# Optimization experiments

Measured on AMD Instinct MI355X. Metric: run time of the kernel, lower is better.

The kernel has to match this reference:

```python
import jax, jax.numpy as jnp
import numpy as np

N = 16384   # nodes
K = 10      # knn_graph(k=11) minus self-loop -> 10 neighbors per node
H = 128     # hidden_nf
L = 7       # n_layers
IN = 8      # in_node_nf
OUT = 4     # out_node_nf


def setup_inputs() -> dict:
    key = jax.random.key(0)
    ks = jax.random.split(key, 20)
    s = 0.05
    rn = lambda k, shp, sc=s: (jax.random.normal(k, shp, dtype=jnp.float32) * sc)
    return {
        "h": jax.random.normal(ks[0], (N, 3 + IN), dtype=jnp.float32) * 100.0,  # cols 0:3 coords (divided by 3330 inside), 3: features
        "idx": jax.random.randint(ks[1], (N, K), 0, N),  # neighbor (src) indices per dst node
        "emb_in_w": rn(ks[2], (IN, H)), "emb_in_b": rn(ks[3], (H,)),
        "edge_w1": rn(ks[4], (L, 2 * H + 1, H)), "edge_b1": rn(ks[5], (L, H)),
        "edge_w2": rn(ks[6], (L, H, H)), "edge_b2": rn(ks[7], (L, H)),
        "coord_w1": rn(ks[8], (L, H, H)), "coord_b1": rn(ks[9], (L, H)),
        "coord_w2": rn(ks[10], (L, H, 1), 0.001),  # xavier gain=0.001, no bias
        "node_w1": rn(ks[11], (L, 2 * H, H)), "node_b1": rn(ks[12], (L, H)),
        "node_w2": rn(ks[13], (L, H, H)), "node_b2": rn(ks[14], (L, H)),
        "emb_out_w": rn(ks[15], (H + 3, OUT)), "emb_out_b": rn(ks[16], (OUT,)),
        "step_count": 0,
    }


def reference(h, idx, emb_in_w, emb_in_b, edge_w1, edge_b1, edge_w2, edge_b2,
              coord_w1, coord_b1, coord_w2, node_w1, node_b1, node_w2, node_b2,
              emb_out_w, emb_out_b, step_count):
    silu = jax.nn.silu
    x = h[:, :3] / 3330.0                       # [N,3] coordinates
    hh = h[:, 3:] @ emb_in_w + emb_in_b         # [N,H] embedding_in (plain Linear)
    for l in range(edge_w1.shape[0]):           # 7 E_GCL layers (structurally distinct params)
        # --- RelativePositionCordMessage (per-edge, edges = (idx[i,k] -> i)) ---
        x_s = x[idx]                            # [N,K,3] src coords (gather)
        hh_s = hh[idx]                          # [N,K,H] src features (gather)
        diff = x_s - x[:, None, :]              # src - dst
        radial = jnp.sum(diff * diff, axis=-1, keepdims=True)   # [N,K,1]
        hh_d = jnp.broadcast_to(hh[:, None, :], hh_s.shape)
        ef = jnp.concatenate([radial, hh_s, hh_d], axis=-1)     # [N,K,2H+1]
        ef = silu(ef @ edge_w1[l] + edge_b1[l])
        ef = silu(ef @ edge_w2[l] + edge_b2[l])                 # edge_feature [N,K,H]
        cm = silu(ef @ coord_w1[l] + coord_b1[l]) @ coord_w2[l] # [N,K,1] (no bias, no tanh)
        trans = diff * cm                                        # [N,K,3]
        # --- Aggregationlayer (mailbox mean/sum reduce + node MLP) ---
        trans = jnp.clip(trans, -1000.0, 1000.0)
        x = jnp.clip(x, -1000.0, 1000.0) + jnp.mean(trans, axis=1)
        agg = jnp.concatenate([hh, jnp.sum(ef, axis=1)], axis=-1)  # [N,2H]
        dh = silu(agg @ node_w1[l] + node_b1[l]) @ node_w2[l] + node_b2[l]
        hh = hh + dh                                              # residual=True
    out = jnp.concatenate([hh, x], axis=-1) @ emb_out_w + emb_out_b  # embedding_out [N,4]
    return out
```

## Files before the change

### kernel.cpp

```cpp
#include <hip/hip_runtime.h>
#include <hip/hip_bf16.h>

#define NN 16384
#define KNN 10
#define HD 128
#define NL 7
#define TM 8
#define EDG 80

#define W1E_OFF 0
#define W1D_OFF 16384
#define W2_OFF  32768
#define C1_OFF  49152
#define N1_OFF  65536
#define N2_OFF  98304
#define WL_STRIDE 114688

typedef float fv4 __attribute__((ext_vector_type(4)));
typedef short bv8 __attribute__((ext_vector_type(8)));

static __device__ __forceinline__ unsigned short f2b(float f) {
  __hip_bfloat16 h = __float2bfloat16(f);
  return __builtin_bit_cast(unsigned short, h);
}
static __device__ __forceinline__ float b2f(unsigned short u) {
  unsigned int x = ((unsigned int)u) << 16;
  return __builtin_bit_cast(float, x);
}
static __device__ __forceinline__ unsigned int pk2(float lo, float hi) {
  unsigned int r;
  asm("v_cvt_pk_bf16_f32 %0, %1, %2" : "=v"(r) : "v"(lo), "v"(hi));
  return r;
}
static __device__ __forceinline__ float silu_f(float x) {
  return x * __builtin_amdgcn_rcpf(1.0f + __expf(-x));
}
#define MFMA(a,b,c) __builtin_amdgcn_mfma_f32_16x16x32_bf16((a),(b),(c),0,0,0)

#define GLOAD_LDS(gp, lp) \
  __builtin_amdgcn_global_load_lds((const __attribute__((address_space(1))) void*)(gp), \
                                   (__attribute__((address_space(3))) void*)(lp), 16, 0, 0)

static __device__ __forceinline__ int swz8(int row, int col) {
  return row * 128 + (col ^ ((row & 7) << 3));
}

__global__ void prep_kernel(const float* __restrict__ ew1, const float* __restrict__ ew2,
                            const float* __restrict__ cw1, const float* __restrict__ nw1,
                            const float* __restrict__ nw2, unsigned short* __restrict__ wt)
{
  int g = blockIdx.x * 256 + threadIdx.x;
  if (g >= NL * WL_STRIDE) return;
  int l = g / WL_STRIDE;
  int r = g % WL_STRIDE;
  float v;
  if (r < 16384) {
    int c = r >> 7, k = r & 127;
    v = ew1[(l*257 + 1 + k)*128 + c];
  } else if (r < 32768) {
    int q = r - 16384; int c = q >> 7, k = q & 127;
    v = ew1[(l*257 + 129 + k)*128 + c];
  } else if (r < 49152) {
    int q = r - 32768; int c = q >> 7, k = q & 127;
    v = ew2[(l*128 + k)*128 + c];
  } else if (r < 65536) {
    int q = r - 49152; int c = q >> 7, k = q & 127;
    v = cw1[(l*128 + k)*128 + c];
  } else if (r < 98304) {
    int q = r - 65536; int c = q >> 8, k = q & 255;
    v = nw1[(l*256 + k)*128 + c];
  } else {
    int q = r - 98304; int c = q >> 7, k = q & 127;
    v = nw2[(l*128 + k)*128 + c];
  }
  wt[g] = f2b(v);
}

__global__ void init_kernel(const float* __restrict__ h, const float* __restrict__ eiw,
                            const float* __restrict__ eib,
                            unsigned short* __restrict__ hhb, float* __restrict__ x)
{
  int g = blockIdx.x * 256 + threadIdx.x;
  int n = g >> 7, c = g & 127;
  float acc = eib[c];
  #pragma unroll
  for (int j = 0; j < 8; ++j) acc += h[n*11 + 3 + j] * eiw[j*128 + c];
  hhb[g] = f2b(acc);
  if (c < 3) x[n*4 + c] = h[n*11 + c] * (1.0f/3330.0f);
  if (c == 3) x[n*4 + 3] = 0.f;
}

__global__ void out_kernel(const unsigned short* __restrict__ hhb, const float* __restrict__ x,
                           const float* __restrict__ ow, const float* __restrict__ ob,
                           float* __restrict__ out)
{
  __shared__ float sOW[131*4];
  int tid = threadIdx.x;
  for (int i = tid; i < 131*4; i += 256) sOW[i] = ow[i];
  __syncthreads();
  int g = blockIdx.x * 256 + tid;
  int n = g >> 2, o = g & 3;
  float acc = ob[o];
  #pragma unroll
  for (int kk = 0; kk < 16; ++kk) {
    bv8 v = *(const bv8*)(hhb + n*128 + kk*8);
    #pragma unroll
    for (int j = 0; j < 8; ++j)
      acc += b2f((unsigned short)v[j]) * sOW[(kk*8 + j)*4 + o];
  }
  #pragma unroll
  for (int d = 0; d < 3; ++d) acc += x[n*4 + d] * sOW[(128 + d)*4 + o];
  out[g] = acc;
}

static __device__ __forceinline__ void load_w8(bv8* w, const unsigned short* __restrict__ W,
                                               int cwb, int lr, int lh) {
  #pragma unroll
  for (int ks = 0; ks < 4; ++ks) {
    w[ks]     = *(const bv8*)(W + (cwb      + lr)*128 + ks*32 + lh*8);
    w[4 + ks] = *(const bv8*)(W + (cwb + 16 + lr)*128 + ks*32 + lh*8);
  }
}

__global__ __launch_bounds__(256, 3) void layer_kernel(
    const int* __restrict__ idxp,
    const unsigned short* __restrict__ wt,
    const float* __restrict__ eb1, const float* __restrict__ eb2,
    const float* __restrict__ cb1, const float* __restrict__ cw2,
    const float* __restrict__ nb1, const float* __restrict__ nb2,
    const float* __restrict__ w1r0p,
    const unsigned short* __restrict__ hhbin,
    unsigned short* __restrict__ hhbout,
    const float* __restrict__ xin, float* __restrict__ xout)
{
  __shared__ __align__(16) unsigned char smem[49792];
  unsigned short* sA   = (unsigned short*)(smem);
  unsigned short* sB   = (unsigned short*)(smem + 20480);
  float*          sHC  = (float*)(smem + 40960);
  unsigned short* sAg  = (unsigned short*)(smem + 45184);
  float*          sCmP = (float*)(smem + 47232);
  float* sRad = (float*)(smem + 48512);
  float* sDx  = (float*)(smem + 48832);
  float* sDy  = (float*)(smem + 49152);
  float* sDz  = (float*)(smem + 49472);
  unsigned short* sEf = sA;
  unsigned short* sN1 = sB;

  const int tid  = threadIdx.x;
  const int wave = tid >> 6;
  const int lane = tid & 63;
  const int lr   = lane & 15;
  const int lh   = lane >> 4;
  const int cwb  = wave * 32;
  const int cb0  = cwb + lh*4;
  const int node0 = blockIdx.x * TM;

  #pragma unroll
  for (int it = 0; it < 5; ++it) {
    int q = tid + it*256;
    int e = q >> 4, cq = q & 15;
    int s = idxp[node0*KNN + e];
    int csw = (cq ^ (e & 7)) << 3;
    GLOAD_LDS(hhbin + s*HD + csw, sA + ((q & ~63) << 3));
  }

  bv8 hb[4];
  #pragma unroll
  for (int ks = 0; ks < 4; ++ks)
    hb[ks] = *(const bv8*)(hhbin + (node0 + (lr & 7))*HD + ks*32 + lh*8);
  bv8 wd[8]; load_w8(wd, wt + W1D_OFF, cwb, lr, lh);
  fv4 cw2v0 = *(const fv4*)(cw2 + cb0);
  fv4 cw2v1 = *(const fv4*)(cw2 + cb0 + 16);
  fv4 w1r0v0 = *(const fv4*)(w1r0p + cb0);
  fv4 w1r0v1 = *(const fv4*)(w1r0p + cb0 + 16);

  if (tid < EDG) {
    int e = tid, n = e / KNN;
    int s = idxp[node0*KNN + e];
    fv4 xs4 = *(const fv4*)(xin + s*4);
    fv4 xd4 = *(const fv4*)(xin + (node0+n)*4);
    float d0 = xs4[0]-xd4[0], d1 = xs4[1]-xd4[1], d2 = xs4[2]-xd4[2];
    sDx[e] = d0; sDy[e] = d1; sDz[e] = d2;
    sRad[e] = d0*d0 + d1*d1 + d2*d2;
  }
  {
    fv4 hac[2];
    hac[0] = *(const fv4*)(eb1 + cb0);
    hac[1] = *(const fv4*)(eb1 + cb0 + 16);
    #pragma unroll
    for (int ks = 0; ks < 4; ++ks) {
      hac[0] = MFMA(wd[ks],   hb[ks], hac[0]);
      hac[1] = MFMA(wd[4+ks], hb[ks], hac[1]);
    }
    if (lr < TM) {
      *(fv4*)(sHC + lr*132 + cb0)      = hac[0];
      *(fv4*)(sHC + lr*132 + cb0 + 16) = hac[1];
    }
  }
  bv8 we[8]; load_w8(we, wt + W1E_OFF, cwb, lr, lh);
  __syncthreads();

  bv8 w2r[8]; load_w8(w2r, wt + W2_OFF, cwb, lr, lh);
  {
    fv4 acc[5][2];
    #pragma unroll
    for (int n = 0; n < 5; ++n) {
      int e = n*16 + lr;
      int nd = e / KNN;
      float rad = sRad[e];
      fv4 h0 = *(const fv4*)(sHC + nd*132 + cb0);
      fv4 h1 = *(const fv4*)(sHC + nd*132 + cb0 + 16);
      acc[n][0] = h0 + w1r0v0*rad;
      acc[n][1] = h1 + w1r0v1*rad;
    }
    #pragma unroll
    for (int ks = 0; ks < 4; ++ks) {
      #pragma unroll
      for (int n = 0; n < 5; ++n) {
        bv8 b = *(const bv8*)(sA + swz8(n*16 + lr, ks*32 + lh*8));
        acc[n][0] = MFMA(we[ks],   b, acc[n][0]);
        acc[n][1] = MFMA(we[4+ks], b, acc[n][1]);
      }
    }
    #pragma unroll
    for (int n = 0; n < 5; ++n) {
      int e = n*16 + lr;
      #pragma unroll
      for (int mt = 0; mt < 2; ++mt) {
        uint2 p;
        p.x = pk2(silu_f(acc[n][mt][0]), silu_f(acc[n][mt][1]));
        p.y = pk2(silu_f(acc[n][mt][2]), silu_f(acc[n][mt][3]));
        *(uint2*)(sB + swz8(e, cb0 + mt*16)) = p;
      }
    }
  }
  __syncthreads();

  bv8 c1r[8]; load_w8(c1r, wt + C1_OFF, cwb, lr, lh);
  {
    fv4 bb0 = *(const fv4*)(eb2 + cb0);
    fv4 bb1 = *(const fv4*)(eb2 + cb0 + 16);
    fv4 acc[5][2];
    #pragma unroll
    for (int n = 0; n < 5; ++n) { acc[n][0] = bb0; acc[n][1] = bb1; }
    #pragma unroll
    for (int ks = 0; ks < 4; ++ks) {
      #pragma unroll
      for (int n = 0; n < 5; ++n) {
        bv8 b = *(const bv8*)(sB + swz8(n*16 + lr, ks*32 + lh*8));
        acc[n][0] = MFMA(w2r[ks],   b, acc[n][0]);
        acc[n][1] = MFMA(w2r[4+ks], b, acc[n][1]);
      }
    }
    #pragma unroll
    for (int n = 0; n < 5; ++n) {
      int e = n*16 + lr;
      #pragma unroll
      for (int mt = 0; mt < 2; ++mt) {
        uint2 p;
        p.x = pk2(silu_f(acc[n][mt][0]), silu_f(acc[n][mt][1]));
        p.y = pk2(silu_f(acc[n][mt][2]), silu_f(acc[n][mt][3]));
        *(uint2*)(sA + swz8(e, cb0 + mt*16)) = p;
      }
    }
  }
  __syncthreads();

  bv8 n1r[16];
  #pragma unroll
  for (int ks = 0; ks < 8; ++ks)
    n1r[ks] = *(const bv8*)(wt + N1_OFF + (cwb + lr)*256 + ks*32 + lh*8);
  {
    fv4 bb0 = *(const fv4*)(cb1 + cb0);
    fv4 bb1 = *(const fv4*)(cb1 + cb0 + 16);
    fv4 acc[5][2];
    #pragma unroll
    for (int n = 0; n < 5; ++n) { acc[n][0] = bb0; acc[n][1] = bb1; }
    #pragma unroll
    for (int ks = 0; ks < 4; ++ks) {
      #pragma unroll
      for (int n = 0; n < 5; ++n) {
        bv8 b = *(const bv8*)(sEf + swz8(n*16 + lr, ks*32 + lh*8));
        acc[n][0] = MFMA(c1r[ks],   b, acc[n][0]);
        acc[n][1] = MFMA(c1r[4+ks], b, acc[n][1]);
      }
    }
    if (tid >= 128) {
      int q = tid - 128;
      int n = q >> 4, c = (q & 15) << 3;
      float s[8] = {0,0,0,0,0,0,0,0};
      #pragma unroll
      for (int k = 0; k < KNN; ++k) {
        bv8 v = *(const bv8*)(sEf + swz8(n*KNN + k, c));
        #pragma unroll
        for (int e8 = 0; e8 < 8; ++e8) s[e8] += b2f((unsigned short)v[e8]);
      }
      uint4 pv = make_uint4(pk2(s[0], s[1]), pk2(s[2], s[3]),
                            pk2(s[4], s[5]), pk2(s[6], s[7]));
      *(uint4*)(sAg + swz8(n, c)) = pv;
    }
    #pragma unroll
    for (int ks = 0; ks < 8; ++ks)
      n1r[8 + ks] = *(const bv8*)(wt + N1_OFF + (cwb + 16 + lr)*256 + ks*32 + lh*8);
    #pragma unroll
    for (int n = 0; n < 5; ++n) {
      float pm = 0.f;
      #pragma unroll
      for (int j = 0; j < 4; ++j) {
        pm += silu_f(acc[n][0][j]) * cw2v0[j];
        pm += silu_f(acc[n][1][j]) * cw2v1[j];
      }
      pm += __shfl_xor(pm, 16);
      pm += __shfl_xor(pm, 32);
      if (lane < 16) sCmP[wave*80 + n*16 + lr] = pm;
    }
  }
  __syncthreads();

  bv8 n2r[8]; load_w8(n2r, wt + N2_OFF, cwb, lr, lh);
  uint2 hres[2];
  if (lr < TM) {
    hres[0] = *(const uint2*)(hhbin + (node0 + lr)*HD + cb0);
    hres[1] = *(const uint2*)(hhbin + (node0 + lr)*HD + cb0 + 16);
  }
  {
    fv4 acc[2];
    acc[0] = *(const fv4*)(nb1 + cb0);
    acc[1] = *(const fv4*)(nb1 + cb0 + 16);
    #pragma unroll
    for (int ks = 0; ks < 8; ++ks) {
      bv8 b = (ks < 4) ? hb[ks]
                       : *(const bv8*)(sAg + swz8(lr & 7, (ks-4)*32 + lh*8));
      acc[0] = MFMA(n1r[ks],   b, acc[0]);
      acc[1] = MFMA(n1r[8+ks], b, acc[1]);
    }
    if (wave == 0) {
      if (lane < 3*TM) {
        int n = lane / 3, d = lane % 3;
        const float* sD = (d == 0) ? sDx : (d == 1) ? sDy : sDz;
        float xo = xin[(node0+n)*4 + d];
        xo = fminf(fmaxf(xo, -1000.f), 1000.f);
        float s = 0.f;
        #pragma unroll
        for (int k = 0; k < KNN; ++k) {
          int e = n*KNN + k;
          float cm = sCmP[e] + sCmP[80 + e] + sCmP[160 + e] + sCmP[240 + e];
          float tr = sD[e] * cm;
          tr = fminf(fmaxf(tr, -1000.f), 1000.f);
          s += tr;
        }
        xout[(node0+n)*4 + d] = xo + s * (1.0f/KNN);
      } else if (lane < 4*TM) {
        xout[(node0 + lane - 3*TM)*4 + 3] = 0.f;
      }
    }
    #pragma unroll
    for (int mt = 0; mt < 2; ++mt) {
      uint2 p;
      p.x = pk2(silu_f(acc[mt][0]), silu_f(acc[mt][1]));
      p.y = pk2(silu_f(acc[mt][2]), silu_f(acc[mt][3]));
      *(uint2*)(sN1 + swz8(lr, cb0 + mt*16)) = p;
    }
  }
  __syncthreads();

  {
    fv4 acc[2];
    acc[0] = *(const fv4*)(nb2 + cb0);
    acc[1] = *(const fv4*)(nb2 + cb0 + 16);
    #pragma unroll
    for (int ks = 0; ks < 4; ++ks) {
      bv8 b = *(const bv8*)(sN1 + swz8(lr, ks*32 + lh*8));
      acc[0] = MFMA(n2r[ks],   b, acc[0]);
      acc[1] = MFMA(n2r[4+ks], b, acc[1]);
    }
    if (lr < TM) {
      #pragma unroll
      for (int mt = 0; mt < 2; ++mt) {
        int g = (node0 + lr)*HD + cb0 + mt*16;
        float v0 = b2f((unsigned short)(hres[mt].x))       + acc[mt][0];
        float v1 = b2f((unsigned short)(hres[mt].x >> 16)) + acc[mt][1];
        float v2 = b2f((unsigned short)(hres[mt].y))       + acc[mt][2];
        float v3 = b2f((unsigned short)(hres[mt].y >> 16)) + acc[mt][3];
        uint2 p;
        p.x = pk2(v0, v1);
        p.y = pk2(v2, v3);
        *(uint2*)(hhbout + g) = p;
      }
    }
  }
}

extern "C" void kernel_launch(void* const* d_in, const int* in_sizes, int n_in,
                              void* d_out, int out_size, void* d_ws, size_t ws_size,
                              hipStream_t stream)
{
  (void)in_sizes; (void)n_in; (void)out_size; (void)ws_size;
  const float* h   = (const float*)d_in[0];
  const int*   idx = (const int*)d_in[1];
  const float* eiw = (const float*)d_in[2];
  const float* eib = (const float*)d_in[3];
  const float* ew1 = (const float*)d_in[4];
  const float* eb1 = (const float*)d_in[5];
  const float* ew2 = (const float*)d_in[6];
  const float* eb2 = (const float*)d_in[7];
  const float* cw1 = (const float*)d_in[8];
  const float* cb1 = (const float*)d_in[9];
  const float* cw2 = (const float*)d_in[10];
  const float* nw1 = (const float*)d_in[11];
  const float* nb1 = (const float*)d_in[12];
  const float* nw2 = (const float*)d_in[13];
  const float* nb2 = (const float*)d_in[14];
  const float* eow = (const float*)d_in[15];
  const float* eob = (const float*)d_in[16];

  unsigned char* ws = (unsigned char*)d_ws;
  unsigned short* wt   = (unsigned short*)ws;
  unsigned short* hhbA = (unsigned short*)(ws + 1605632);
  unsigned short* hhbB = (unsigned short*)(ws + 5799936);
  float*          xA   = (float*)(ws + 9994240);
  float*          xB   = (float*)(ws + 10256384);

  prep_kernel<<<(NL*WL_STRIDE + 255)/256, 256, 0, stream>>>(ew1, ew2, cw1, nw1, nw2, wt);
  init_kernel<<<NN*HD/256, 256, 0, stream>>>(h, eiw, eib, hhbA, xA);

  unsigned short* hbs = hhbA; unsigned short* hbd = hhbB;
  float* xs = xA; float* xd = xB;
  for (int l = 0; l < NL; ++l) {
    layer_kernel<<<NN/TM, 256, 0, stream>>>(idx, wt + (size_t)l*WL_STRIDE,
        eb1 + l*128, eb2 + l*128, cb1 + l*128, cw2 + l*128,
        nb1 + l*128, nb2 + l*128,
        ew1 + (size_t)l*257*128,
        hbs, hbd, xs, xd);
    unsigned short* ht = hbs; hbs = hbd; hbd = ht;
    float* t = xs; xs = xd; xd = t;
  }
  out_kernel<<<NN*4/256, 256, 0, stream>>>(hbs, xs, eow, eob, (float*)d_out);
}
```

Measured before the change: 474.4 us.

## Compute edge-sum aggregation in registers per wave and drop a block barrier

```diff
diff --git a/kernel.cpp b/kernel.cpp
--- a/kernel.cpp
+++ b/kernel.cpp
@@ -133,16 +133,15 @@
     unsigned short* __restrict__ hhbout,
     const float* __restrict__ xin, float* __restrict__ xout)
 {
-  __shared__ __align__(16) unsigned char smem[49792];
+  __shared__ __align__(16) unsigned char smem[47744];
   unsigned short* sA   = (unsigned short*)(smem);
   unsigned short* sB   = (unsigned short*)(smem + 20480);
   float*          sHC  = (float*)(smem + 40960);
-  unsigned short* sAg  = (unsigned short*)(smem + 45184);
-  float*          sCmP = (float*)(smem + 47232);
-  float* sRad = (float*)(smem + 48512);
-  float* sDx  = (float*)(smem + 48832);
-  float* sDy  = (float*)(smem + 49152);
-  float* sDz  = (float*)(smem + 49472);
+  float*          sCmP = (float*)(smem + 45184);
+  float* sRad = (float*)(smem + 46464);
+  float* sDx  = (float*)(smem + 46784);
+  float* sDy  = (float*)(smem + 47104);
+  float* sDz  = (float*)(smem + 47424);
   unsigned short* sEf = sA;
   unsigned short* sN1 = sB;
 
@@ -155,13 +154,16 @@
   const int cb0  = cwb + lh*4;
   const int node0 = blockIdx.x * TM;
 
+  int Ireg = 0;
+  if (lane < 20)
+    Ireg = idxp[node0*KNN + 4*wave + (lane & 3) + 16*(lane >> 2)];
+
   #pragma unroll
   for (int it = 0; it < 5; ++it) {
-    int q = tid + it*256;
-    int e = q >> 4, cq = q & 15;
-    int s = idxp[node0*KNN + e];
-    int csw = (cq ^ (e & 7)) << 3;
-    GLOAD_LDS(hhbin + s*HD + csw, sA + ((q & ~63) << 3));
+    int s = __shfl(Ireg, 4*it + (lane >> 4));
+    int e = 4*wave + (lane >> 4) + 16*it;
+    int csw = ((lane & 15) ^ (e & 7)) << 3;
+    GLOAD_LDS(hhbin + s*HD + csw, sA + (((tid & ~63) + it*256) << 3));
   }
 
   bv8 hb[4];
@@ -266,10 +268,6 @@
   }
   __syncthreads();
 
-  bv8 n1r[16];
-  #pragma unroll
-  for (int ks = 0; ks < 8; ++ks)
-    n1r[ks] = *(const bv8*)(wt + N1_OFF + (cwb + lr)*256 + ks*32 + lh*8);
   {
     fv4 bb0 = *(const fv4*)(cb1 + cb0);
     fv4 bb1 = *(const fv4*)(cb1 + cb0 + 16);
@@ -285,23 +283,6 @@
         acc[n][1] = MFMA(c1r[4+ks], b, acc[n][1]);
       }
     }
-    if (tid >= 128) {
-      int q = tid - 128;
-      int n = q >> 4, c = (q & 15) << 3;
-      float s[8] = {0,0,0,0,0,0,0,0};
-      #pragma unroll
-      for (int k = 0; k < KNN; ++k) {
-        bv8 v = *(const bv8*)(sEf + swz8(n*KNN + k, c));
-        #pragma unroll
-        for (int e8 = 0; e8 < 8; ++e8) s[e8] += b2f((unsigned short)v[e8]);
-      }
-      uint4 pv = make_uint4(pk2(s[0], s[1]), pk2(s[2], s[3]),
-                            pk2(s[4], s[5]), pk2(s[6], s[7]));
-      *(uint4*)(sAg + swz8(n, c)) = pv;
-    }
-    #pragma unroll
-    for (int ks = 0; ks < 8; ++ks)
-      n1r[8 + ks] = *(const bv8*)(wt + N1_OFF + (cwb + 16 + lr)*256 + ks*32 + lh*8);
     #pragma unroll
     for (int n = 0; n < 5; ++n) {
       float pm = 0.f;
@@ -315,8 +296,49 @@
       if (lane < 16) sCmP[wave*80 + n*16 + lr] = pm;
     }
   }
-  __syncthreads();
-
+  bv8 n1r[16];
+  #pragma unroll
+  for (int ks = 0; ks < 8; ++ks) {
+    n1r[ks]     = *(const bv8*)(wt + N1_OFF + (cwb      + lr)*256 + ks*32 + lh*8);
+    n1r[8 + ks] = *(const bv8*)(wt + N1_OFF + (cwb + 16 + lr)*256 + ks*32 + lh*8);
+  }
+  bv8 agb[4];
+  {
+    int nd = lr & 7;
+    int tsel = (lane & 8) ? 2 : 0;
+    unsigned int pkv[2][4];
+    #pragma unroll
+    for (int t = 0; t < 2; ++t) {
+      int c = (tsel + t)*32 + lh*8;
+      float s0=0,s1=0,s2=0,s3=0,s4=0,s5=0,s6=0,s7=0;
+      #pragma unroll
+      for (int k = 0; k < KNN; ++k) {
+        bv8 v = *(const bv8*)(sEf + swz8(nd*KNN + k, c));
+        s0 += b2f((unsigned short)v[0]); s1 += b2f((unsigned short)v[1]);
+        s2 += b2f((unsigned short)v[2]); s3 += b2f((unsigned short)v[3]);
+        s4 += b2f((unsigned short)v[4]); s5 += b2f((unsigned short)v[5]);
+        s6 += b2f((unsigned short)v[6]); s7 += b2f((unsigned short)v[7]);
+      }
+      pkv[t][0] = pk2(s0, s1); pkv[t][1] = pk2(s2, s3);
+      pkv[t][2] = pk2(s4, s5); pkv[t][3] = pk2(s6, s7);
+    }
+    unsigned int rcv[2][4];
+    #pragma unroll
+    for (int t = 0; t < 2; ++t)
+      #pragma unroll
+      for (int j = 0; j < 4; ++j)
+        rcv[t][j] = (unsigned int)__shfl_xor((int)pkv[t][j], 8);
+    union { unsigned int u[4]; bv8 v; } cv;
+    #pragma unroll
+    for (int t = 0; t < 2; ++t) {
+      #pragma unroll
+      for (int j = 0; j < 4; ++j) cv.u[j] = (lane & 8) ? rcv[t][j] : pkv[t][j];
+      agb[t] = cv.v;
+      #pragma unroll
+      for (int j = 0; j < 4; ++j) cv.u[j] = (lane & 8) ? pkv[t][j] : rcv[t][j];
+      agb[2 + t] = cv.v;
+    }
+  }
   bv8 n2r[8]; load_w8(n2r, wt + N2_OFF, cwb, lr, lh);
   uint2 hres[2];
   if (lr < TM) {
@@ -329,10 +351,29 @@
     acc[1] = *(const fv4*)(nb1 + cb0 + 16);
     #pragma unroll
     for (int ks = 0; ks < 8; ++ks) {
-      bv8 b = (ks < 4) ? hb[ks]
-                       : *(const bv8*)(sAg + swz8(lr & 7, (ks-4)*32 + lh*8));
+      bv8 b = (ks < 4) ? hb[ks] : agb[ks - 4];
       acc[0] = MFMA(n1r[ks],   b, acc[0]);
       acc[1] = MFMA(n1r[8+ks], b, acc[1]);
+    }
+    #pragma unroll
+    for (int mt = 0; mt < 2; ++mt) {
+      uint2 p;
+      p.x = pk2(silu_f(acc[mt][0]), silu_f(acc[mt][1]));
+      p.y = pk2(silu_f(acc[mt][2]), silu_f(acc[mt][3]));
+      *(uint2*)(sN1 + swz8(lr, cb0 + mt*16)) = p;
+    }
+  }
+  __syncthreads();
+
+  {
+    fv4 acc[2];
+    acc[0] = *(const fv4*)(nb2 + cb0);
+    acc[1] = *(const fv4*)(nb2 + cb0 + 16);
+    #pragma unroll
+    for (int ks = 0; ks < 4; ++ks) {
+      bv8 b = *(const bv8*)(sN1 + swz8(lr, ks*32 + lh*8));
+      acc[0] = MFMA(n2r[ks],   b, acc[0]);
+      acc[1] = MFMA(n2r[4+ks], b, acc[1]);
     }
     if (wave == 0) {
       if (lane < 3*TM) {
@@ -353,26 +394,6 @@
       } else if (lane < 4*TM) {
         xout[(node0 + lane - 3*TM)*4 + 3] = 0.f;
       }
-    }
-    #pragma unroll
-    for (int mt = 0; mt < 2; ++mt) {
-      uint2 p;
-      p.x = pk2(silu_f(acc[mt][0]), silu_f(acc[mt][1]));
-      p.y = pk2(silu_f(acc[mt][2]), silu_f(acc[mt][3]));
-      *(uint2*)(sN1 + swz8(lr, cb0 + mt*16)) = p;
-    }
-  }
-  __syncthreads();
-
-  {
-    fv4 acc[2];
-    acc[0] = *(const fv4*)(nb2 + cb0);
-    acc[1] = *(const fv4*)(nb2 + cb0 + 16);
-    #pragma unroll
-    for (int ks = 0; ks < 4; ++ks) {
-      bv8 b = *(const bv8*)(sN1 + swz8(lr, ks*32 + lh*8));
-      acc[0] = MFMA(n2r[ks],   b, acc[0]);
-      acc[1] = MFMA(n2r[4+ks], b, acc[1]);
     }
     if (lr < TM) {
       #pragma unroll
```

Measured after the change: 493.1 us. 1.04x slower.

## Split layer kernel into edge kernel and 64-node node-MLP kernel

Applied to the files above, without the earlier changes.

```diff
diff --git a/kernel.cpp b/kernel.cpp
--- a/kernel.cpp
+++ b/kernel.cpp
@@ -7,6 +7,7 @@
 #define NL 7
 #define TM 8
 #define EDG 80
+#define NE (NN*KNN)
 
 #define W1E_OFF 0
 #define W1D_OFF 16384
@@ -122,29 +123,24 @@
   }
 }
 
-__global__ __launch_bounds__(256, 3) void layer_kernel(
+__global__ __launch_bounds__(256, 3) void edge_kernel(
     const int* __restrict__ idxp,
     const unsigned short* __restrict__ wt,
     const float* __restrict__ eb1, const float* __restrict__ eb2,
     const float* __restrict__ cb1, const float* __restrict__ cw2,
-    const float* __restrict__ nb1, const float* __restrict__ nb2,
     const float* __restrict__ w1r0p,
     const unsigned short* __restrict__ hhbin,
-    unsigned short* __restrict__ hhbout,
-    const float* __restrict__ xin, float* __restrict__ xout)
-{
-  __shared__ __align__(16) unsigned char smem[49792];
+    const float* __restrict__ xin,
+    unsigned short* __restrict__ aggg,
+    float* __restrict__ diffg,
+    float* __restrict__ cmPg)
+{
+  __shared__ __align__(16) unsigned char smem[45504];
   unsigned short* sA   = (unsigned short*)(smem);
   unsigned short* sB   = (unsigned short*)(smem + 20480);
   float*          sHC  = (float*)(smem + 40960);
-  unsigned short* sAg  = (unsigned short*)(smem + 45184);
-  float*          sCmP = (float*)(smem + 47232);
-  float* sRad = (float*)(smem + 48512);
-  float* sDx  = (float*)(smem + 48832);
-  float* sDy  = (float*)(smem + 49152);
-  float* sDz  = (float*)(smem + 49472);
+  float*          sRad = (float*)(smem + 45184);
   unsigned short* sEf = sA;
-  unsigned short* sN1 = sB;
 
   const int tid  = threadIdx.x;
   const int wave = tid >> 6;
@@ -180,8 +176,10 @@
     fv4 xs4 = *(const fv4*)(xin + s*4);
     fv4 xd4 = *(const fv4*)(xin + (node0+n)*4);
     float d0 = xs4[0]-xd4[0], d1 = xs4[1]-xd4[1], d2 = xs4[2]-xd4[2];
-    sDx[e] = d0; sDy[e] = d1; sDz[e] = d2;
-    sRad[e] = d0*d0 + d1*d1 + d2*d2;
+    float rad = d0*d0 + d1*d1 + d2*d2;
+    sRad[e] = rad;
+    fv4 dv = (fv4){d0, d1, d2, rad};
+    *(fv4*)(diffg + (node0*KNN + e)*4) = dv;
   }
   {
     fv4 hac[2];
@@ -266,10 +264,6 @@
   }
   __syncthreads();
 
-  bv8 n1r[16];
-  #pragma unroll
-  for (int ks = 0; ks < 8; ++ks)
-    n1r[ks] = *(const bv8*)(wt + N1_OFF + (cwb + lr)*256 + ks*32 + lh*8);
   {
     fv4 bb0 = *(const fv4*)(cb1 + cb0);
     fv4 bb1 = *(const fv4*)(cb1 + cb0 + 16);
@@ -285,6 +279,18 @@
         acc[n][1] = MFMA(c1r[4+ks], b, acc[n][1]);
       }
     }
+    #pragma unroll
+    for (int n = 0; n < 5; ++n) {
+      float pm = 0.f;
+      #pragma unroll
+      for (int j = 0; j < 4; ++j) {
+        pm += silu_f(acc[n][0][j]) * cw2v0[j];
+        pm += silu_f(acc[n][1][j]) * cw2v1[j];
+      }
+      pm += __shfl_xor(pm, 16);
+      pm += __shfl_xor(pm, 32);
+      if (lane < 16) cmPg[wave*NE + node0*KNN + n*16 + lr] = pm;
+    }
     if (tid >= 128) {
       int q = tid - 128;
       int n = q >> 4, c = (q & 15) << 3;
@@ -297,96 +303,128 @@
       }
       uint4 pv = make_uint4(pk2(s[0], s[1]), pk2(s[2], s[3]),
                             pk2(s[4], s[5]), pk2(s[6], s[7]));
-      *(uint4*)(sAg + swz8(n, c)) = pv;
-    }
-    #pragma unroll
-    for (int ks = 0; ks < 8; ++ks)
-      n1r[8 + ks] = *(const bv8*)(wt + N1_OFF + (cwb + 16 + lr)*256 + ks*32 + lh*8);
-    #pragma unroll
-    for (int n = 0; n < 5; ++n) {
-      float pm = 0.f;
-      #pragma unroll
-      for (int j = 0; j < 4; ++j) {
-        pm += silu_f(acc[n][0][j]) * cw2v0[j];
-        pm += silu_f(acc[n][1][j]) * cw2v1[j];
-      }
-      pm += __shfl_xor(pm, 16);
-      pm += __shfl_xor(pm, 32);
-      if (lane < 16) sCmP[wave*80 + n*16 + lr] = pm;
-    }
-  }
-  __syncthreads();
-
-  bv8 n2r[8]; load_w8(n2r, wt + N2_OFF, cwb, lr, lh);
-  uint2 hres[2];
-  if (lr < TM) {
-    hres[0] = *(const uint2*)(hhbin + (node0 + lr)*HD + cb0);
-    hres[1] = *(const uint2*)(hhbin + (node0 + lr)*HD + cb0 + 16);
-  }
-  {
-    fv4 acc[2];
-    acc[0] = *(const fv4*)(nb1 + cb0);
-    acc[1] = *(const fv4*)(nb1 + cb0 + 16);
-    #pragma unroll
-    for (int ks = 0; ks < 8; ++ks) {
-      bv8 b = (ks < 4) ? hb[ks]
-                       : *(const bv8*)(sAg + swz8(lr & 7, (ks-4)*32 + lh*8));
-      acc[0] = MFMA(n1r[ks],   b, acc[0]);
-      acc[1] = MFMA(n1r[8+ks], b, acc[1]);
-    }
-    if (wave == 0) {
-      if (lane < 3*TM) {
-        int n = lane / 3, d = lane % 3;
-        const float* sD = (d == 0) ? sDx : (d == 1) ? sDy : sDz;
-        float xo = xin[(node0+n)*4 + d];
-        xo = fminf(fmaxf(xo, -1000.f), 1000.f);
-        float s = 0.f;
-        #pragma unroll
-        for (int k = 0; k < KNN; ++k) {
-          int e = n*KNN + k;
-          float cm = sCmP[e] + sCmP[80 + e] + sCmP[160 + e] + sCmP[240 + e];
-          float tr = sD[e] * cm;
-          tr = fminf(fmaxf(tr, -1000.f), 1000.f);
-          s += tr;
-        }
-        xout[(node0+n)*4 + d] = xo + s * (1.0f/KNN);
-      } else if (lane < 4*TM) {
-        xout[(node0 + lane - 3*TM)*4 + 3] = 0.f;
-      }
-    }
-    #pragma unroll
-    for (int mt = 0; mt < 2; ++mt) {
+      *(uint4*)(aggg + (node0 + n)*HD + c) = pv;
+    }
+  }
+}
+
+__global__ __launch_bounds__(256, 3) void node_kernel(
+    const unsigned short* __restrict__ wt,
+    const float* __restrict__ nb1, const float* __restrict__ nb2,
+    const unsigned short* __restrict__ hhbin,
+    const unsigned short* __restrict__ aggg,
+    const float* __restrict__ diffg,
+    const float* __restrict__ cmPg,
+    const float* __restrict__ xin, float* __restrict__ xout,
+    unsigned short* __restrict__ hhbout)
+{
+  __shared__ __align__(16) unsigned char smem[49152];
+  unsigned short* sIn0 = (unsigned short*)(smem);
+  unsigned short* sIn1 = (unsigned short*)(smem + 16384);
+  unsigned short* sN1  = (unsigned short*)(smem + 32768);
+
+  const int tid  = threadIdx.x;
+  const int lane = tid & 63;
+  const int wave = tid >> 6;
+  const int lr   = lane & 15;
+  const int lh   = lane >> 4;
+  const int cwb  = wave * 32;
+  const int cb0  = cwb + lh*4;
+  const int node0 = blockIdx.x * 64;
+
+  #pragma unroll
+  for (int it = 0; it < 4; ++it) {
+    int q = tid + it*256;
+    int r = q >> 4, cq = q & 15;
+    int csw = (cq ^ (r & 7)) << 3;
+    GLOAD_LDS(hhbin + (node0 + r)*HD + csw, sIn0 + ((q & ~63) << 3));
+  }
+  #pragma unroll
+  for (int it = 0; it < 4; ++it) {
+    int q = tid + it*256;
+    int r = q >> 4, cq = q & 15;
+    int csw = (cq ^ (r & 7)) << 3;
+    GLOAD_LDS(aggg + (node0 + r)*HD + csw, sIn1 + ((q & ~63) << 3));
+  }
+  bv8 n1r[16];
+  #pragma unroll
+  for (int ks = 0; ks < 8; ++ks) {
+    n1r[ks]     = *(const bv8*)(wt + N1_OFF + (cwb      + lr)*256 + ks*32 + lh*8);
+    n1r[8 + ks] = *(const bv8*)(wt + N1_OFF + (cwb + 16 + lr)*256 + ks*32 + lh*8);
+  }
+  if (tid < 192) {
+    int n = tid / 3, d = tid % 3;
+    int e0 = (node0 + n)*KNN;
+    float xo = xin[(node0+n)*4 + d];
+    xo = fminf(fmaxf(xo, -1000.f), 1000.f);
+    float s = 0.f;
+    #pragma unroll
+    for (int k = 0; k < KNN; ++k) {
+      int e = e0 + k;
+      float cm = cmPg[e] + cmPg[NE + e] + cmPg[2*NE + e] + cmPg[3*NE + e];
+      float tr = diffg[e*4 + d] * cm;
+      tr = fminf(fmaxf(tr, -1000.f), 1000.f);
+      s += tr;
+    }
+    xout[(node0+n)*4 + d] = xo + s * (1.0f/KNN);
+  }
+  __syncthreads();
+
+  {
+    fv4 bb0 = *(const fv4*)(nb1 + cb0);
+    fv4 bb1 = *(const fv4*)(nb1 + cb0 + 16);
+    #pragma unroll
+    for (int t = 0; t < 4; ++t) {
+      fv4 acc0 = bb0, acc1 = bb1;
+      #pragma unroll
+      for (int ks = 0; ks < 4; ++ks) {
+        bv8 b0 = *(const bv8*)(sIn0 + swz8(t*16 + lr, ks*32 + lh*8));
+        bv8 b1 = *(const bv8*)(sIn1 + swz8(t*16 + lr, ks*32 + lh*8));
+        acc0 = MFMA(n1r[ks],      b0, acc0);
+        acc0 = MFMA(n1r[4+ks],    b1, acc0);
+        acc1 = MFMA(n1r[8+ks],    b0, acc1);
+        acc1 = MFMA(n1r[12+ks],   b1, acc1);
+      }
+      uint2 p0, p1;
+      p0.x = pk2(silu_f(acc0[0]), silu_f(acc0[1]));
+      p0.y = pk2(silu_f(acc0[2]), silu_f(acc0[3]));
+      p1.x = pk2(silu_f(acc1[0]), silu_f(acc1[1]));
+      p1.y = pk2(silu_f(acc1[2]), silu_f(acc1[3]));
+      *(uint2*)(sN1 + swz8(t*16 + lr, cb0))      = p0;
+      *(uint2*)(sN1 + swz8(t*16 + lr, cb0 + 16)) = p1;
+    }
+  }
+  __syncthreads();
+
+  {
+    bv8 n2r[8]; load_w8(n2r, wt + N2_OFF, cwb, lr, lh);
+    fv4 bb0 = *(const fv4*)(nb2 + cb0);
+    fv4 bb1 = *(const fv4*)(nb2 + cb0 + 16);
+    #pragma unroll
+    for (int t = 0; t < 4; ++t) {
+      fv4 acc0 = bb0, acc1 = bb1;
+      #pragma unroll
+      for (int ks = 0; ks < 4; ++ks) {
+        bv8 b = *(const bv8*)(sN1 + swz8(t*16 + lr, ks*32 + lh*8));
+        acc0 = MFMA(n2r[ks],   b, acc0);
+        acc1 = MFMA(n2r[4+ks], b, acc1);
+      }
+      uint2 r0 = *(const uint2*)(sIn0 + swz8(t*16 + lr, cb0));
+      uint2 r1 = *(const uint2*)(sIn0 + swz8(t*16 + lr, cb0 + 16));
+      float v0 = b2f((unsigned short)(r0.x))       + acc0[0];
+      float v1 = b2f((unsigned short)(r0.x >> 16)) + acc0[1];
+      float v2 = b2f((unsigned short)(r0.y))       + acc0[2];
+      float v3 = b2f((unsigned short)(r0.y >> 16)) + acc0[3];
+      float w0 = b2f((unsigned short)(r1.x))       + acc1[0];
+      float w1 = b2f((unsigned short)(r1.x >> 16)) + acc1[1];
+      float w2 = b2f((unsigned short)(r1.y))       + acc1[2];
+      float w3 = b2f((unsigned short)(r1.y >> 16)) + acc1[3];
+      int g = (node0 + t*16 + lr)*HD + cb0;
       uint2 p;
-      p.x = pk2(silu_f(acc[mt][0]), silu_f(acc[mt][1]));
-      p.y = pk2(silu_f(acc[mt][2]), silu_f(acc[mt][3]));
-      *(uint2*)(sN1 + swz8(lr, cb0 + mt*16)) = p;
-    }
-  }
-  __syncthreads();
-
-  {
-    fv4 acc[2];
-    acc[0] = *(const fv4*)(nb2 + cb0);
-    acc[1] = *(const fv4*)(nb2 + cb0 + 16);
-    #pragma unroll
-    for (int ks = 0; ks < 4; ++ks) {
-      bv8 b = *(const bv8*)(sN1 + swz8(lr, ks*32 + lh*8));
-      acc[0] = MFMA(n2r[ks],   b, acc[0]);
-      acc[1] = MFMA(n2r[4+ks], b, acc[1]);
-    }
-    if (lr < TM) {
-      #pragma unroll
-      for (int mt = 0; mt < 2; ++mt) {
-        int g = (node0 + lr)*HD + cb0 + mt*16;
-        float v0 = b2f((unsigned short)(hres[mt].x))       + acc[mt][0];
-        float v1 = b2f((unsigned short)(hres[mt].x >> 16)) + acc[mt][1];
-        float v2 = b2f((unsigned short)(hres[mt].y))       + acc[mt][2];
-        float v3 = b2f((unsigned short)(hres[mt].y >> 16)) + acc[mt][3];
-        uint2 p;
-        p.x = pk2(v0, v1);
-        p.y = pk2(v2, v3);
-        *(uint2*)(hhbout + g) = p;
-      }
+      p.x = pk2(v0, v1); p.y = pk2(v2, v3);
+      *(uint2*)(hhbout + g) = p;
+      p.x = pk2(w0, w1); p.y = pk2(w2, w3);
+      *(uint2*)(hhbout + g + 16) = p;
     }
   }
 }
@@ -415,11 +453,14 @@
   const float* eob = (const float*)d_in[16];
 
   unsigned char* ws = (unsigned char*)d_ws;
-  unsigned short* wt   = (unsigned short*)ws;
-  unsigned short* hhbA = (unsigned short*)(ws + 1605632);
-  unsigned short* hhbB = (unsigned short*)(ws + 5799936);
-  float*          xA   = (float*)(ws + 9994240);
-  float*          xB   = (float*)(ws + 10256384);
+  unsigned short* wt    = (unsigned short*)ws;
+  unsigned short* hhbA  = (unsigned short*)(ws + 1605632);
+  unsigned short* hhbB  = (unsigned short*)(ws + 5799936);
+  float*          xA    = (float*)(ws + 9994240);
+  float*          xB    = (float*)(ws + 10256384);
+  unsigned short* aggg  = (unsigned short*)(ws + 10518528);
+  float*          diffg = (float*)(ws + 14712832);
+  float*          cmPg  = (float*)(ws + 17334272);
 
   prep_kernel<<<(NL*WL_STRIDE + 255)/256, 256, 0, stream>>>(ew1, ew2, cw1, nw1, nw2, wt);
   init_kernel<<<NN*HD/256, 256, 0, stream>>>(h, eiw, eib, hhbA, xA);
@@ -427,11 +468,13 @@
   unsigned short* hbs = hhbA; unsigned short* hbd = hhbB;
   float* xs = xA; float* xd = xB;
   for (int l = 0; l < NL; ++l) {
-    layer_kernel<<<NN/TM, 256, 0, stream>>>(idx, wt + (size_t)l*WL_STRIDE,
+    edge_kernel<<<NN/TM, 256, 0, stream>>>(idx, wt + (size_t)l*WL_STRIDE,
         eb1 + l*128, eb2 + l*128, cb1 + l*128, cw2 + l*128,
+        ew1 + (size_t)l*257*128,
+        hbs, xs, aggg, diffg, cmPg);
+    node_kernel<<<NN/64, 256, 0, stream>>>(wt + (size_t)l*WL_STRIDE,
         nb1 + l*128, nb2 + l*128,
-        ew1 + (size_t)l*257*128,
-        hbs, hbd, xs, xd);
+        hbs, aggg, diffg, cmPg, xs, xd, hbd);
     unsigned short* ht = hbs; hbs = hbd; hbd = ht;
     float* t = xs; xs = xd; xd = t;
   }
```

After: 394.8 us. 16.8% less time.
